# Kernel optimization log

Measured on AMD Instinct MI355X. Metric: run time of the kernel, lower is better.

## Reference

```python
import jax, jax.numpy as jnp
import numpy as np

B, L, D, H = 8, 1024, 1024, 16
HD = D // H  # head dim = 64


def _split_heads(x):
    # [B, L, D] -> [B, H, L, HD]
    return x.reshape(B, L, H, HD).transpose(0, 2, 1, 3)


def setup_inputs() -> dict:
    key = jax.random.key(0)
    ks = jax.random.split(key, 16)
    s = 0.02
    inp = {
        "hidden_states": jax.random.normal(ks[0], (B, L, D), jnp.float32),
        "attention_mask": jnp.zeros((B, 1, 1, L), jnp.float32),
        "source_embedding": jax.random.normal(ks[1], (B, L, D), jnp.float32),
        # self-attention projections
        "Wq": jax.random.normal(ks[2], (D, D), jnp.float32) * s,
        "bq": jnp.zeros((D,), jnp.float32),
        "Wk": jax.random.normal(ks[3], (D, D), jnp.float32) * s,
        "bk": jnp.zeros((D,), jnp.float32),
        "Wv": jax.random.normal(ks[4], (D, D), jnp.float32) * s,
        "bv": jnp.zeros((D,), jnp.float32),
        # SourceAttendsSubthread projections (query on hidden, key on source)
        "Wq2": jax.random.normal(ks[5], (D, D), jnp.float32) * s,
        "bq2": jnp.zeros((D,), jnp.float32),
        "Wk2": jax.random.normal(ks[6], (D, D), jnp.float32) * s,
        "bk2": jnp.zeros((D,), jnp.float32),
    }
    return inp


def reference(hidden_states, attention_mask, source_embedding,
              Wq, bq, Wk, bk, Wv, bv, Wq2, bq2, Wk2, bk2):
    scale = 1.0 / jnp.sqrt(jnp.asarray(HD, hidden_states.dtype))
    q = _split_heads(hidden_states @ Wq + bq)          # [B,H,L,HD]
    k = _split_heads(hidden_states @ Wk + bk)
    v = _split_heads(hidden_states @ Wv + bv)
    q2 = _split_heads(hidden_states @ Wq2 + bq2)
    k2 = _split_heads(source_embedding @ Wk2 + bk2)
    scores = jnp.einsum('bhqd,bhkd->bhqk', q, k) * scale
    scores = scores + jnp.einsum('bhqd,bhkd->bhqk', q2, k2) * scale
    scores = scores + attention_mask                   # broadcast [B,1,1,L]
    probs = jax.nn.softmax(scores, axis=-1)            # dropout is identity (p=0 / eval)
    ctx = jnp.einsum('bhqk,bhkd->bhqd', probs, v)      # [B,H,L,HD]
    return ctx.transpose(0, 2, 1, 3).reshape(B, L, D)
```

## Files before the change

kernel.cpp:

```cpp
#include <hip/hip_runtime.h>
#include <hip/hip_bf16.h>
#include <stdint.h>

#define Bn 8
#define Ln 1024
#define Dn 1024
#define Hn 16
#define HDn 64
#define Mn (Bn*Ln)
#define Kn 1024

typedef __attribute__((ext_vector_type(8))) __bf16 bf16x8;
typedef __attribute__((ext_vector_type(4))) float f32x4;

__device__ __forceinline__ unsigned short f2bf(float f) {
    unsigned int u = __float_as_uint(f);
    unsigned int r = (u + 0x7fff + ((u >> 16) & 1)) >> 16;
    return (unsigned short)r;
}

__device__ __forceinline__ void gload_lds16(void* lds, const void* g) {
    __builtin_amdgcn_global_load_lds(
        (const __attribute__((address_space(1))) unsigned int*)g,
        (__attribute__((address_space(3))) unsigned int*)lds,
        16, 0, 0);
}

__global__ void prep_kernel(const float* __restrict__ h,
                            const float* __restrict__ s,
                            const float* __restrict__ Wq,
                            const float* __restrict__ Wk,
                            const float* __restrict__ Wq2,
                            const float* __restrict__ Wk2,
                            const float* __restrict__ Wv,
                            unsigned short* __restrict__ ho,
                            unsigned short* __restrict__ so,
                            unsigned short* __restrict__ wcat4,
                            unsigned short* __restrict__ wtv) {
    __shared__ float tile[32][33];
    int bid = blockIdx.x;
    int t = threadIdx.x;
    if (bid < 16384) {
        const float* in = (bid >> 13) ? s : h;
        unsigned short* out = (bid >> 13) ? so : ho;
        size_t i = (((size_t)(bid & 8191)) * 256 + t) * 4;
        float4 f = *(const float4*)(in + i);
        ushort4 o;
        o.x = f2bf(f.x); o.y = f2bf(f.y); o.z = f2bf(f.z); o.w = f2bf(f.w);
        *(ushort4*)(out + i) = o;
        return;
    }
    int bid2 = bid - 16384;
    int z = bid2 >> 10, tl = bid2 & 1023;
    int bx = tl & 31, by = tl >> 5;
    const float* W; unsigned short* Wt;
    switch (z) {
        case 0: W = Wq;  Wt = wcat4;                 break;
        case 1: W = Wk;  Wt = wcat4 + 1024 * 1024;   break;
        case 2: W = Wq2; Wt = wcat4 + 2048 * 1024;   break;
        case 3: W = Wk2; Wt = wcat4 + 3072 * 1024;   break;
        default:W = Wv;  Wt = wtv;                   break;
    }
    int tx = t & 31, ty = t >> 5;
    int col = bx * 32 + tx;
    for (int i = 0; i < 32; i += 8)
        tile[ty + i][tx] = W[(size_t)(by * 32 + ty + i) * Dn + col];
    __syncthreads();
    int ok = by * 32 + tx;
    for (int i = 0; i < 32; i += 8)
        Wt[(size_t)(bx * 32 + ty + i) * Kn + ok] = f2bf(tile[tx][ty + i]);
}

__device__ __forceinline__ void gemm_mainloop(const unsigned short* __restrict__ A,
                                              const unsigned short* __restrict__ Bt,
                                              unsigned short* As, unsigned short* Bs,
                                              int m0, int n0, f32x4 acc[4][4]) {
    int t = threadIdx.x;
    int lane = t & 63, wave = t >> 6;
    int wm = (wave >> 1) * 64, wn = (wave & 1) * 64;
    int lrow = lane & 15, lquad = lane >> 4;

    int srow = t >> 3;
    int sc8 = ((t & 7) ^ (srow & 7)) * 8;
    const unsigned short* ap = A  + (size_t)(m0 + srow) * Kn + sc8;
    const unsigned short* bp = Bt + (size_t)(n0 + srow) * Kn + sc8;
    int rph = lrow & 7;

    for (int k0 = 0; k0 < Kn; k0 += 64) {
        for (int s = 0; s < 4; s++) {
            gload_lds16(&As[(t + 256 * s) * 8], ap + (size_t)(32 * s) * Kn + k0);
            gload_lds16(&Bs[(t + 256 * s) * 8], bp + (size_t)(32 * s) * Kn + k0);
        }
        __syncthreads();
        for (int kk = 0; kk < 2; kk++) {
            bf16x8 af[4], bfr[4];
            for (int i = 0; i < 4; i++)
                af[i] = *(const bf16x8*)&As[(wm + i * 16 + lrow) * 64 + ((kk * 4 + lquad) ^ rph) * 8];
            for (int j = 0; j < 4; j++)
                bfr[j] = *(const bf16x8*)&Bs[(wn + j * 16 + lrow) * 64 + ((kk * 4 + lquad) ^ rph) * 8];
            for (int i = 0; i < 4; i++)
                for (int j = 0; j < 4; j++)
                    acc[i][j] = __builtin_amdgcn_mfma_f32_16x16x32_bf16(af[i], bfr[j], acc[i][j], 0, 0, 0);
        }
        __syncthreads();
    }
}

__launch_bounds__(256, 3)
__global__ void gemm_all_kernel(const unsigned short* __restrict__ hb,
                                const unsigned short* __restrict__ sb,
                                const unsigned short* __restrict__ wcat4,
                                const unsigned short* __restrict__ wtv,
                                const float* __restrict__ bq,
                                const float* __restrict__ bk,
                                const float* __restrict__ bq2,
                                const float* __restrict__ bk2,
                                const float* __restrict__ bv,
                                unsigned short* __restrict__ qbuf,
                                unsigned short* __restrict__ kbuf,
                                unsigned short* __restrict__ q2buf,
                                unsigned short* __restrict__ k2buf,
                                unsigned short* __restrict__ vtbuf) {
    __shared__ __align__(16) unsigned short As[128 * 64];
    __shared__ __align__(16) unsigned short Bs[128 * 64];
    int bid = blockIdx.x;
    int t = threadIdx.x;
    int lane = t & 63, wave = t >> 6;
    int wm = (wave >> 1) * 64, wn = (wave & 1) * 64;
    int lrow = lane & 15, lquad = lane >> 4;
    f32x4 acc[4][4] = {};

    if (bid < 2048) {
        int n0 = (bid & 31) * 128, m0 = (bid >> 5) * 128;
        int region = n0 >> 10;
        const unsigned short* A = (region == 3) ? sb : hb;
        gemm_mainloop(A, wcat4, As, Bs, m0, n0, acc);

        const float* bp = region == 0 ? bq : region == 1 ? bk : region == 2 ? bq2 : bk2;
        unsigned short* dp = region == 0 ? qbuf : region == 1 ? kbuf : region == 2 ? q2buf : k2buf;
        float sc = (region == 0 || region == 2) ? 0.125f : 1.0f;
        for (int j = 0; j < 4; j++) {
            int gn = (n0 & 1023) + wn + j * 16 + lrow;
            float bv_ = bp[gn];
            int h = gn >> 6, hd = gn & 63;
            for (int i = 0; i < 4; i++)
                for (int r = 0; r < 4; r++) {
                    int gm = m0 + wm + i * 16 + lquad * 4 + r;
                    int b = gm >> 10, ll = gm & 1023;
                    dp[((size_t)(b * Hn + h) * Ln + ll) * HDn + hd] = f2bf((acc[i][j][r] + bv_) * sc);
                }
        }
    } else {
        int b2 = bid - 2048;
        int n0 = (b2 & 63) * 128;
        int m0 = (b2 >> 6) * 128;
        gemm_mainloop(wtv, hb, As, Bs, m0, n0, acc);

        for (int j = 0; j < 4; j++) {
            int gn = n0 + wn + j * 16 + lrow;
            int b = gn >> 10, l = gn & 1023;
            for (int i = 0; i < 4; i++)
                for (int r = 0; r < 4; r++) {
                    int gm = m0 + wm + i * 16 + lquad * 4 + r;
                    int h = gm >> 6, hd = gm & 63;
                    vtbuf[((size_t)(b * Hn + h) * HDn + hd) * Ln + l] = f2bf(acc[i][j][r] + bv[gm]);
                }
        }
    }
}

__launch_bounds__(256, 3)
__global__ void attn_kernel(const unsigned short* __restrict__ qb,
                            const unsigned short* __restrict__ kb,
                            const unsigned short* __restrict__ q2b,
                            const unsigned short* __restrict__ k2b,
                            const unsigned short* __restrict__ vtb,
                            const float* __restrict__ mask,
                            float* __restrict__ out) {
    __shared__ __align__(16) unsigned short Ks[64 * 64];
    __shared__ __align__(16) unsigned short K2s[64 * 64];
    __shared__ __align__(16) unsigned short VTs[64 * 64];
    __shared__ __align__(16) unsigned short Ps[4 * 32 * 64];

    int bh = blockIdx.x;
    int qt = blockIdx.y;
    int b = bh >> 4;
    int t = threadIdx.x;
    int lane = t & 63, wave = t >> 6;
    int lrow = lane & 15, lquad = lane >> 4;
    int qbase = qt * 128 + wave * 32;

    bf16x8 qf[2][2], q2f[2][2];
    for (int rt = 0; rt < 2; rt++)
        for (int kk = 0; kk < 2; kk++) {
            size_t off = ((size_t)bh * Ln + qbase + rt * 16 + lrow) * HDn + kk * 32 + lquad * 8;
            qf[rt][kk]  = *(const bf16x8*)(qb + off);
            q2f[rt][kk] = *(const bf16x8*)(q2b + off);
        }

    f32x4 O[2][4] = {};
    f32x4 lsum[2] = {};

    int srow = t >> 3;
    int sc8 = ((t & 7) ^ (srow & 7)) * 8;
    const float* maskb = mask + (size_t)b * Ln;
    int rph = lrow & 7;
    unsigned short* pw = &Ps[wave * 32 * 64];

    for (int kt = 0; kt < 16; kt++) {
        int key0 = kt * 64;
        gload_lds16(&Ks[t * 8],          kb  + ((size_t)bh * Ln + key0 + srow) * HDn + sc8);
        gload_lds16(&Ks[(t + 256) * 8],  kb  + ((size_t)bh * Ln + key0 + 32 + srow) * HDn + sc8);
        gload_lds16(&K2s[t * 8],         k2b + ((size_t)bh * Ln + key0 + srow) * HDn + sc8);
        gload_lds16(&K2s[(t + 256) * 8], k2b + ((size_t)bh * Ln + key0 + 32 + srow) * HDn + sc8);
        gload_lds16(&VTs[t * 8],         vtb + ((size_t)bh * HDn + srow) * Ln + key0 + sc8);
        gload_lds16(&VTs[(t + 256) * 8], vtb + ((size_t)bh * HDn + 32 + srow) * Ln + key0 + sc8);
        __syncthreads();

        f32x4 S[2][4];
        for (int j = 0; j < 4; j++) {
            float mk = maskb[key0 + j * 16 + lrow];
            S[0][j] = (f32x4){mk, mk, mk, mk};
            S[1][j] = S[0][j];
        }
        for (int kk = 0; kk < 2; kk++) {
            for (int j = 0; j < 4; j++) {
                bf16x8 kf = *(const bf16x8*)&Ks[(j * 16 + lrow) * 64 + ((kk * 4 + lquad) ^ rph) * 8];
                S[0][j] = __builtin_amdgcn_mfma_f32_16x16x32_bf16(qf[0][kk], kf, S[0][j], 0, 0, 0);
                S[1][j] = __builtin_amdgcn_mfma_f32_16x16x32_bf16(qf[1][kk], kf, S[1][j], 0, 0, 0);
            }
            for (int j = 0; j < 4; j++) {
                bf16x8 kf = *(const bf16x8*)&K2s[(j * 16 + lrow) * 64 + ((kk * 4 + lquad) ^ rph) * 8];
                S[0][j] = __builtin_amdgcn_mfma_f32_16x16x32_bf16(q2f[0][kk], kf, S[0][j], 0, 0, 0);
                S[1][j] = __builtin_amdgcn_mfma_f32_16x16x32_bf16(q2f[1][kk], kf, S[1][j], 0, 0, 0);
            }
        }

        for (int rt = 0; rt < 2; rt++)
            for (int j = 0; j < 4; j++)
                for (int r = 0; r < 4; r++) {
                    float e = __expf(S[rt][j][r]);
                    lsum[rt][r] += e;
                    int pr = rt * 16 + lquad * 4 + r;
                    int cw = (j * 2 + (lrow >> 3)) ^ (pr & 7);
                    pw[pr * 64 + cw * 8 + (lrow & 7)] = f2bf(e);
                }

        for (int kk = 0; kk < 2; kk++) {
            bf16x8 pf0 = *(const bf16x8*)&pw[lrow * 64 + ((kk * 4 + lquad) ^ rph) * 8];
            bf16x8 pf1 = *(const bf16x8*)&pw[(16 + lrow) * 64 + ((kk * 4 + lquad) ^ rph) * 8];
            for (int j = 0; j < 4; j++) {
                bf16x8 vf = *(const bf16x8*)&VTs[(j * 16 + lrow) * 64 + ((kk * 4 + lquad) ^ rph) * 8];
                O[0][j] = __builtin_amdgcn_mfma_f32_16x16x32_bf16(pf0, vf, O[0][j], 0, 0, 0);
                O[1][j] = __builtin_amdgcn_mfma_f32_16x16x32_bf16(pf1, vf, O[1][j], 0, 0, 0);
            }
        }
        __syncthreads();
    }

    for (int rt = 0; rt < 2; rt++)
        for (int r = 0; r < 4; r++) {
            float s = lsum[rt][r];
            for (int d = 1; d < 16; d <<= 1)
                s += __shfl_xor(s, d, 64);
            lsum[rt][r] = s;
        }

    int h = bh & 15;
    for (int rt = 0; rt < 2; rt++)
        for (int r = 0; r < 4; r++) {
            float rl = 1.0f / lsum[rt][r];
            int ql = qbase + rt * 16 + lquad * 4 + r;
            for (int j = 0; j < 4; j++)
                out[((size_t)b * Ln + ql) * Dn + h * HDn + j * 16 + lrow] = O[rt][j][r] * rl;
        }
}

extern "C" void kernel_launch(void* const* d_in, const int* in_sizes, int n_in,
                              void* d_out, int out_size, void* d_ws, size_t ws_size,
                              hipStream_t stream) {
    const float* hidden = (const float*)d_in[0];
    const float* mask   = (const float*)d_in[1];
    const float* source = (const float*)d_in[2];
    const float* Wq  = (const float*)d_in[3];
    const float* bq  = (const float*)d_in[4];
    const float* Wk  = (const float*)d_in[5];
    const float* bk  = (const float*)d_in[6];
    const float* Wv  = (const float*)d_in[7];
    const float* bv  = (const float*)d_in[8];
    const float* Wq2 = (const float*)d_in[9];
    const float* bq2 = (const float*)d_in[10];
    const float* Wk2 = (const float*)d_in[11];
    const float* bk2 = (const float*)d_in[12];
    float* out = (float*)d_out;

    char* ws = (char*)d_ws;
    const size_t act_sz = (size_t)Mn * Dn * 2;
    const size_t w_sz   = (size_t)Kn * Dn * 2;
    unsigned short* hb    = (unsigned short*)ws; ws += act_sz;
    unsigned short* sb    = (unsigned short*)ws; ws += act_sz;
    unsigned short* wcat4 = (unsigned short*)ws; ws += 4 * w_sz;
    unsigned short* wtv   = (unsigned short*)ws; ws += w_sz;
    unsigned short* qbuf  = (unsigned short*)ws; ws += act_sz;
    unsigned short* kbuf  = (unsigned short*)ws; ws += act_sz;
    unsigned short* q2buf = (unsigned short*)ws; ws += act_sz;
    unsigned short* k2buf = (unsigned short*)ws; ws += act_sz;
    unsigned short* vtbuf = (unsigned short*)ws; ws += act_sz;

    prep_kernel<<<21504, 256, 0, stream>>>(hidden, source, Wq, Wk, Wq2, Wk2, Wv,
                                           hb, sb, wcat4, wtv);

    gemm_all_kernel<<<2560, 256, 0, stream>>>(hb, sb, wcat4, wtv,
                                              bq, bk, bq2, bk2, bv,
                                              qbuf, kbuf, q2buf, k2buf, vtbuf);

    dim3 agrid(Bn * Hn, Ln / 128);
    attn_kernel<<<agrid, 256, 0, stream>>>(qbuf, kbuf, q2buf, k2buf, vtbuf, mask, out);
}
```

Measured before the change: 340.3 us.

## Compute transposed scores so P stays in registers and skips the LDS round trip

The QK^T MFMAs now run with swapped operands so each lane holds S^T fragments. Those fragments map directly onto the B operand of a 16x16x16 bf16 MFMA for the PV product, so the per-wave LDS buffer for P and its scattered stores and reloads are gone. V^T is read as 4-element fragments, the row sum needs only two cross-quad shuffles, and output is written as float4. The cost is twice as many smaller MFMAs (16x16x16 instead of 16x16x32) for PV.

```diff
diff --git a/kernel.cpp b/kernel.cpp
--- a/kernel.cpp
+++ b/kernel.cpp
@@ -11,12 +11,22 @@
 #define Kn 1024
 
 typedef __attribute__((ext_vector_type(8))) __bf16 bf16x8;
+typedef __attribute__((ext_vector_type(4))) __bf16 bf16x4;
+typedef __attribute__((ext_vector_type(4))) short s16x4;
 typedef __attribute__((ext_vector_type(4))) float f32x4;
 
 __device__ __forceinline__ unsigned short f2bf(float f) {
     unsigned int u = __float_as_uint(f);
     unsigned int r = (u + 0x7fff + ((u >> 16) & 1)) >> 16;
     return (unsigned short)r;
+}
+
+__device__ __forceinline__ f32x4 mfma16_bf16(bf16x4 a, s16x4 b, f32x4 c) {
+#if __has_builtin(__builtin_amdgcn_mfma_f32_16x16x16_bf16)
+    return __builtin_amdgcn_mfma_f32_16x16x16_bf16(a, __builtin_bit_cast(bf16x4, b), c, 0, 0, 0);
+#else
+    return __builtin_amdgcn_mfma_f32_16x16x16bf16_1k(__builtin_bit_cast(s16x4, a), b, c, 0, 0, 0);
+#endif
 }
 
 __device__ __forceinline__ void gload_lds16(void* lds, const void* g) {
@@ -180,32 +190,30 @@
     __shared__ __align__(16) unsigned short Ks[64 * 64];
     __shared__ __align__(16) unsigned short K2s[64 * 64];
     __shared__ __align__(16) unsigned short VTs[64 * 64];
-    __shared__ __align__(16) unsigned short Ps[4 * 32 * 64];
 
     int bh = blockIdx.x;
     int qt = blockIdx.y;
     int b = bh >> 4;
     int t = threadIdx.x;
     int lane = t & 63, wave = t >> 6;
-    int lrow = lane & 15, lquad = lane >> 4;
+    int lrow = lane & 15, quad = lane >> 4;
     int qbase = qt * 128 + wave * 32;
 
     bf16x8 qf[2][2], q2f[2][2];
     for (int rt = 0; rt < 2; rt++)
         for (int kk = 0; kk < 2; kk++) {
-            size_t off = ((size_t)bh * Ln + qbase + rt * 16 + lrow) * HDn + kk * 32 + lquad * 8;
+            size_t off = ((size_t)bh * Ln + qbase + rt * 16 + lrow) * HDn + kk * 32 + quad * 8;
             qf[rt][kk]  = *(const bf16x8*)(qb + off);
             q2f[rt][kk] = *(const bf16x8*)(q2b + off);
         }
 
-    f32x4 O[2][4] = {};
-    f32x4 lsum[2] = {};
+    f32x4 O[4][2] = {};
+    float lsum[2] = {0.f, 0.f};
 
     int srow = t >> 3;
     int sc8 = ((t & 7) ^ (srow & 7)) * 8;
     const float* maskb = mask + (size_t)b * Ln;
     int rph = lrow & 7;
-    unsigned short* pw = &Ps[wave * 32 * 64];
 
     for (int kt = 0; kt < 16; kt++) {
         int key0 = kt * 64;
@@ -217,63 +225,61 @@
         gload_lds16(&VTs[(t + 256) * 8], vtb + ((size_t)bh * HDn + 32 + srow) * Ln + key0 + sc8);
         __syncthreads();
 
-        f32x4 S[2][4];
+        f32x4 SJ[4][2];
         for (int j = 0; j < 4; j++) {
-            float mk = maskb[key0 + j * 16 + lrow];
-            S[0][j] = (f32x4){mk, mk, mk, mk};
-            S[1][j] = S[0][j];
+            float4 mk = *(const float4*)(maskb + key0 + j * 16 + quad * 4);
+            SJ[j][0] = (f32x4){mk.x, mk.y, mk.z, mk.w};
+            SJ[j][1] = SJ[j][0];
         }
         for (int kk = 0; kk < 2; kk++) {
             for (int j = 0; j < 4; j++) {
-                bf16x8 kf = *(const bf16x8*)&Ks[(j * 16 + lrow) * 64 + ((kk * 4 + lquad) ^ rph) * 8];
-                S[0][j] = __builtin_amdgcn_mfma_f32_16x16x32_bf16(qf[0][kk], kf, S[0][j], 0, 0, 0);
-                S[1][j] = __builtin_amdgcn_mfma_f32_16x16x32_bf16(qf[1][kk], kf, S[1][j], 0, 0, 0);
+                bf16x8 kf = *(const bf16x8*)&Ks[(j * 16 + lrow) * 64 + ((kk * 4 + quad) ^ rph) * 8];
+                SJ[j][0] = __builtin_amdgcn_mfma_f32_16x16x32_bf16(kf, qf[0][kk], SJ[j][0], 0, 0, 0);
+                SJ[j][1] = __builtin_amdgcn_mfma_f32_16x16x32_bf16(kf, qf[1][kk], SJ[j][1], 0, 0, 0);
             }
             for (int j = 0; j < 4; j++) {
-                bf16x8 kf = *(const bf16x8*)&K2s[(j * 16 + lrow) * 64 + ((kk * 4 + lquad) ^ rph) * 8];
-                S[0][j] = __builtin_amdgcn_mfma_f32_16x16x32_bf16(q2f[0][kk], kf, S[0][j], 0, 0, 0);
-                S[1][j] = __builtin_amdgcn_mfma_f32_16x16x32_bf16(q2f[1][kk], kf, S[1][j], 0, 0, 0);
+                bf16x8 k2 = *(const bf16x8*)&K2s[(j * 16 + lrow) * 64 + ((kk * 4 + quad) ^ rph) * 8];
+                SJ[j][0] = __builtin_amdgcn_mfma_f32_16x16x32_bf16(k2, q2f[0][kk], SJ[j][0], 0, 0, 0);
+                SJ[j][1] = __builtin_amdgcn_mfma_f32_16x16x32_bf16(k2, q2f[1][kk], SJ[j][1], 0, 0, 0);
             }
         }
 
-        for (int rt = 0; rt < 2; rt++)
-            for (int j = 0; j < 4; j++)
+        s16x4 P[4][2];
+        for (int j = 0; j < 4; j++)
+            for (int rt = 0; rt < 2; rt++)
                 for (int r = 0; r < 4; r++) {
-                    float e = __expf(S[rt][j][r]);
-                    lsum[rt][r] += e;
-                    int pr = rt * 16 + lquad * 4 + r;
-                    int cw = (j * 2 + (lrow >> 3)) ^ (pr & 7);
-                    pw[pr * 64 + cw * 8 + (lrow & 7)] = f2bf(e);
+                    float e = __expf(SJ[j][rt][r]);
+                    lsum[rt] += e;
+                    P[j][rt][r] = (short)f2bf(e);
                 }
 
-        for (int kk = 0; kk < 2; kk++) {
-            bf16x8 pf0 = *(const bf16x8*)&pw[lrow * 64 + ((kk * 4 + lquad) ^ rph) * 8];
-            bf16x8 pf1 = *(const bf16x8*)&pw[(16 + lrow) * 64 + ((kk * 4 + lquad) ^ rph) * 8];
+        for (int mb = 0; mb < 4; mb++)
             for (int j = 0; j < 4; j++) {
-                bf16x8 vf = *(const bf16x8*)&VTs[(j * 16 + lrow) * 64 + ((kk * 4 + lquad) ^ rph) * 8];
-                O[0][j] = __builtin_amdgcn_mfma_f32_16x16x32_bf16(pf0, vf, O[0][j], 0, 0, 0);
-                O[1][j] = __builtin_amdgcn_mfma_f32_16x16x32_bf16(pf1, vf, O[1][j], 0, 0, 0);
+                bf16x4 va = *(const bf16x4*)&VTs[(mb * 16 + lrow) * 64 +
+                              ((2 * j + (quad >> 1)) ^ rph) * 8 + (quad & 1) * 4];
+                O[mb][0] = mfma16_bf16(va, P[j][0], O[mb][0]);
+                O[mb][1] = mfma16_bf16(va, P[j][1], O[mb][1]);
             }
-        }
         __syncthreads();
     }
 
-    for (int rt = 0; rt < 2; rt++)
-        for (int r = 0; r < 4; r++) {
-            float s = lsum[rt][r];
-            for (int d = 1; d < 16; d <<= 1)
-                s += __shfl_xor(s, d, 64);
-            lsum[rt][r] = s;
-        }
+    float rl[2];
+    for (int rt = 0; rt < 2; rt++) {
+        float s = lsum[rt];
+        s += __shfl_xor(s, 16, 64);
+        s += __shfl_xor(s, 32, 64);
+        rl[rt] = 1.0f / s;
+    }
 
     int h = bh & 15;
-    for (int rt = 0; rt < 2; rt++)
-        for (int r = 0; r < 4; r++) {
-            float rl = 1.0f / lsum[rt][r];
-            int ql = qbase + rt * 16 + lquad * 4 + r;
-            for (int j = 0; j < 4; j++)
-                out[((size_t)b * Ln + ql) * Dn + h * HDn + j * 16 + lrow] = O[rt][j][r] * rl;
-        }
+    for (int rt = 0; rt < 2; rt++) {
+        int ql = qbase + rt * 16 + lrow;
+        for (int mb = 0; mb < 4; mb++) {
+            float4 o4 = {O[mb][rt][0] * rl[rt], O[mb][rt][1] * rl[rt],
+                         O[mb][rt][2] * rl[rt], O[mb][rt][3] * rl[rt]};
+            *(float4*)(out + ((size_t)b * Ln + ql) * Dn + h * HDn + mb * 16 + quad * 4) = o4;
+        }
+    }
 }
 
 extern "C" void kernel_launch(void* const* d_in, const int* in_sizes, int n_in,
```

After: 319.6 us. -6.1%, faster.
